# Optimization experiments

Hardware: AMD Instinct MI355X
Metric: run time of the kernel (lower is better)

Reference implementation:

```python
import jax, jax.numpy as jnp
import numpy as np

NEG = -100000000.0  # NOT_POSSIBLE_TRANSITION
B, T, F, NT = 64, 512, 1024, 50
H = NT + 2  # +2 for start/stop tags
START, STOP = H - 2, H - 1


def setup_inputs() -> dict:
    key = jax.random.key(0)
    k0, k1, k2, k3 = jax.random.split(key, 4)
    features = jax.random.normal(k0, (B, T, F), jnp.float32)
    tags = jax.random.randint(k1, (B, T), 0, NT)
    masks = jnp.ones((B, T), jnp.float32)
    W = jax.random.normal(k2, (H, F), jnp.float32) * 0.02  # nn.Linear weight
    b = jnp.zeros((H,), jnp.float32)                        # nn.Linear bias
    transition = jax.random.normal(k3, (H, H), jnp.float32)
    transition = transition.at[START, :].set(NEG).at[:, STOP].set(NEG)
    return dict(features=features, W=W, b=b, transition=transition,
                masks=masks, tags=tags)


def _forward_algorithm(emit, masks, transition):
    # emit: [B,T,H], masks: [B,T]
    b_, _, h = emit.shape
    init = jnp.full((b_, h), NEG, emit.dtype).at[:, START].set(0.0)

    def step(scores, xs):
        emit_t, mask_t = xs  # [B,H], [B]
        # score_t[b, i] = logsumexp_j(scores[b,j] + transition[i,j] + emit_t[b,i])
        s = scores[:, None, :] + transition[None, :, :] + emit_t[:, :, None]
        s = jax.nn.logsumexp(s, axis=-1)
        m = mask_t[:, None]
        scores = s * m + scores * (1.0 - m)
        return scores, None

    scores, _ = jax.lax.scan(step, init, (emit.transpose(1, 0, 2), masks.T))
    return jax.nn.logsumexp(scores + transition[STOP], axis=-1)  # [B]


def _gold_score(emit, tags, masks, transition):
    b_ = emit.shape[0]
    emit_sc = jnp.take_along_axis(emit, tags[:, :, None], axis=2)[:, :, 0]  # [B,T]
    start = jnp.full((b_, 1), START, tags.dtype)
    tags_ext = jnp.concatenate([start, tags], axis=1)  # [B,T+1]
    trans_sc = transition[tags_ext[:, 1:], tags_ext[:, :-1]]  # [B,T]
    last_pos = masks.sum(axis=1).astype(jnp.int32)  # index into tags_ext
    last_tag = jnp.take_along_axis(tags_ext, last_pos[:, None], axis=1)[:, 0]
    last_score = transition[STOP, last_tag]
    return ((trans_sc + emit_sc) * masks).sum(axis=1) + last_score  # [B]


def reference(features, W, b, transition, masks, tags):
    emit = features @ W.T + b  # [B,T,H]
    fwd = _forward_algorithm(emit, masks, transition)
    gold = _gold_score(emit, tags, masks, transition)
    return (fwd - gold).mean()  # CRF NLL loss (scalar)


if __name__ == "__main__":
    print(reference(**setup_inputs()))
```

## Files before the change

### kernel.cpp

```cpp
#include <hip/hip_runtime.h>
#include <hip/hip_bf16.h>
#include <math.h>


#define NEGV   (-100000000.0f)
#define BB     64
#define TT     512
#define FF     1024
#define HH     52
#define HP     64
#define S_START 50
#define S_STOP  51
#define NCH    32
#define CLEN   (TT / NCH)

typedef __bf16 bf16x8 __attribute__((ext_vector_type(8)));
typedef __bf16 bf16x4 __attribute__((ext_vector_type(4)));
typedef float  f32x4  __attribute__((ext_vector_type(4)));

#define WS_CHUNK  0u
#define WS_WBF    33554432u
#define WS_EXPT   33685504u
#define WS_GOLD   33693696u
#define WS_CEXP   33693952u

__global__ __launch_bounds__(256) void k_prep(const float* __restrict__ W,
                                              const float* __restrict__ trans,
                                              __bf16* __restrict__ wbf,
                                              __bf16* __restrict__ expT,
                                              float* __restrict__ gold) {
  int n = blockIdx.x;
  if (n == 0) {
    if (threadIdx.x < BB) gold[threadIdx.x] = 0.0f;
    for (int idx = threadIdx.x; idx < 4096; idx += 256) {
      int m = idx >> 6, k = idx & 63;
      float tv = (k >= HH) ? NEGV : ((m >= HH) ? 0.0f : trans[m * HH + k]);
      expT[idx] = (__bf16)__expf(tv);
    }
  }
  for (int k = threadIdx.x; k < FF; k += 256) {
    float v = (n < HH) ? W[n * FF + k] : 0.0f;
    wbf[n * FF + k] = (__bf16)v;
  }
}

__global__ __launch_bounds__(256, 2) void k_scan(const float* __restrict__ feat,
                                                 const __bf16* __restrict__ wbf,
                                                 const __bf16* __restrict__ expT,
                                                 const float* __restrict__ bias,
                                                 const float* __restrict__ trans,
                                                 const float* __restrict__ masks,
                                                 const int* __restrict__ tags,
                                                 float* __restrict__ chunks,
                                                 float* __restrict__ cexp,
                                                 float* __restrict__ gold) {
  const int tid = threadIdx.x;
  const int wv = tid >> 6;
  const int l  = tid & 63;
  const int lm = l & 15;
  const int q  = l >> 4;
  const int chunk = blockIdx.x * 4 + wv;
  const int b = chunk >> 5, c = chunk & 31;

  __shared__ __align__(16) __bf16 PTall[4][64 * 72];
  __shared__ __align__(16) __bf16 Eall[4][CLEN * 64];
  __bf16* pt = PTall[wv];
  __bf16* el = Eall[wv];

  const float* fbase = feat + ((size_t)(b * TT + c * CLEN)) * FF;
  const float* arow  = fbase + (size_t)lm * FF + q * 8;

  f32x4 apre[4][2];
#pragma unroll
  for (int s = 0; s < 4; ++s)
#pragma unroll
    for (int h = 0; h < 2; ++h)
      apre[s][h] = *(const f32x4*)(arow + s * 32 + h * 4);

  bf16x8 bcur[4];
#pragma unroll
  for (int nt = 0; nt < 4; ++nt)
    bcur[nt] = *(const bf16x8*)(wbf + (size_t)(nt * 16 + lm) * FF + q * 8);

  f32x4 acc[4] = {};

#pragma unroll
  for (int kt = 0; kt < 32; ++kt) {
    const int st = kt & 3;
    bf16x8 af;
#pragma unroll
    for (int j = 0; j < 4; ++j) {
      af[j]     = (__bf16)apre[st][0][j];
      af[4 + j] = (__bf16)apre[st][1][j];
    }
    if (kt + 4 < 32) {
#pragma unroll
      for (int h = 0; h < 2; ++h)
        apre[st][h] = *(const f32x4*)(arow + (kt + 4) * 32 + h * 4);
    }
    bf16x8 bnx[4];
    if (kt + 1 < 32) {
#pragma unroll
      for (int nt = 0; nt < 4; ++nt)
        bnx[nt] = *(const bf16x8*)(wbf + (size_t)(nt * 16 + lm) * FF + (kt + 1) * 32 + q * 8);
    }
#pragma unroll
    for (int nt = 0; nt < 4; ++nt)
      acc[nt] = __builtin_amdgcn_mfma_f32_16x16x32_bf16(af, bcur[nt], acc[nt], 0, 0, 0);
    if (kt + 1 < 32) {
#pragma unroll
      for (int nt = 0; nt < 4; ++nt) bcur[nt] = bnx[nt];
    }
  }

#pragma unroll
  for (int nt = 0; nt < 4; ++nt) {
    int n = nt * 16 + lm;
    float bn = (n < HH) ? bias[n] : 0.0f;
#pragma unroll
    for (int rr = 0; rr < 4; ++rr)
      el[(q * 4 + rr) * 64 + n] = (__bf16)(acc[nt][rr] + bn);
  }

  float mreg = (l < CLEN) ? masks[b * TT + c * CLEN + l] : 1.0f;
  int cur = (l < CLEN) ? tags[b * TT + c * CLEN + l] : 0;
  int prev = __shfl_up(cur, 1);
  if (l == 0) prev = (c == 0) ? S_START : tags[b * TT + c * CLEN - 1];
  float gp = 0.0f;
  if (l < CLEN) {
    float e  = (float)el[l * 64 + cur];
    float tr = trans[cur * HH + prev];
    gp = (e + tr) * mreg;
  }
#pragma unroll
  for (int d = 1; d < 64; d <<= 1) gp += __shfl_xor(gp, d);
  if (l == 0) atomicAdd(&gold[b], gp);

  bf16x8 afrag[4][2];
#pragma unroll
  for (int mt = 0; mt < 4; ++mt)
#pragma unroll
    for (int kk = 0; kk < 2; ++kk)
      afrag[mt][kk] = *(const bf16x8*)&expT[(mt * 16 + lm) * 64 + kk * 32 + q * 8];

  for (int idx = l; idx < 4096; idx += 64) {
    int n = idx >> 6, mm = idx & 63;
    pt[n * 72 + mm] = (__bf16)((n == mm) ? 1.0f : 0.0f);
  }

  int eacc = 0, rpend = 0;
  const float LOG2E = 1.4426950408889634f;

  for (int t = 0; t < CLEN; ++t) {
    float mcur = __shfl(mreg, t);
    if (mcur != 0.0f) {
      float sh = (float)(7 + rpend);
      eacc += 7 + rpend;
      rpend = 0;
      float s[4][4];
#pragma unroll
      for (int mt = 0; mt < 4; ++mt) {
        bf16x4 em4 = *(const bf16x4*)&el[t * 64 + mt * 16 + q * 4];
#pragma unroll
        for (int rr = 0; rr < 4; ++rr)
          s[mt][rr] = __builtin_amdgcn_exp2f(fmaf((float)em4[rr], LOG2E, -sh));
      }

      bf16x8 bfr[2][4];
#pragma unroll
      for (int kk = 0; kk < 2; ++kk)
#pragma unroll
        for (int nt = 0; nt < 4; ++nt)
          bfr[kk][nt] = *(const bf16x8*)&pt[(nt * 16 + lm) * 72 + kk * 32 + q * 8];

      const bool trk = ((t & 7) == 7) && (t != CLEN - 1);
      float lmax = 0.0f;
      f32x4 zero = {};
#pragma unroll
      for (int mt = 0; mt < 4; ++mt) {
#pragma unroll
        for (int nt = 0; nt < 4; ++nt) {
          f32x4 a = __builtin_amdgcn_mfma_f32_16x16x32_bf16(afrag[mt][0], bfr[0][nt], zero, 0, 0, 0);
          a = __builtin_amdgcn_mfma_f32_16x16x32_bf16(afrag[mt][1], bfr[1][nt], a, 0, 0, 0);
          bf16x4 w4;
#pragma unroll
          for (int rr = 0; rr < 4; ++rr) {
            float v = a[rr] * s[mt][rr];
            if (trk) lmax = fmaxf(lmax, v);
            w4[rr] = (__bf16)v;
          }
          *(bf16x4*)&pt[(nt * 16 + lm) * 72 + mt * 16 + q * 4] = w4;
        }
      }
      if (trk) {
#pragma unroll
        for (int d = 1; d < 64; d <<= 1) lmax = fmaxf(lmax, __shfl_xor(lmax, d));
        rpend = ilogbf(lmax);
      }
    }
  }

  f32x4* c4 = (f32x4*)(chunks + (size_t)chunk * 4096);
#pragma unroll
  for (int it = 0; it < 16; ++it) {
    f32x4 v;
#pragma unroll
    for (int jr = 0; jr < 4; ++jr) v[jr] = (float)pt[(it * 4 + jr) * 72 + l];
    c4[it * 64 + l] = v;
  }
  if (l == 0) cexp[chunk] = (float)eacc;
}

__global__ __launch_bounds__(64) void k_combine(const float* __restrict__ chunks,
                                                const float* __restrict__ cexp,
                                                const float* __restrict__ trans,
                                                const float* __restrict__ masks,
                                                const int* __restrict__ tags,
                                                const float* __restrict__ gold,
                                                float* __restrict__ out) {
  const int b = blockIdx.x;
  const int l = threadIdx.x;
  __shared__ float vsh[64];
  float v = (l == S_START) ? 1.0f : 0.0f;
  float esum = 0.0f;
  const float LN2 = 0.6931471805599453f;

  float msum = 0.0f;
  for (int t = l; t < TT; t += 64) msum += masks[b * TT + t];

  f32x4 mb[2][16];
  {
    const f32x4* M = (const f32x4*)(chunks + ((size_t)(b * NCH)) * 4096);
#pragma unroll
    for (int jj = 0; jj < 16; ++jj) mb[0][jj] = M[jj * 64 + l];
  }

#pragma unroll
  for (int cc = 0; cc < NCH; ++cc) {
    vsh[l] = v;
    __syncthreads();
    if (cc + 1 < NCH) {
      const f32x4* Mn = (const f32x4*)(chunks + ((size_t)(b * NCH + cc + 1)) * 4096);
#pragma unroll
      for (int jj = 0; jj < 16; ++jj) mb[(cc + 1) & 1][jj] = Mn[jj * 64 + l];
    }
    f32x4 u4 = {};
#pragma unroll
    for (int jj = 0; jj < 16; ++jj) {
      f32x4 m4 = mb[cc & 1][jj];
      const float* vj = &vsh[jj * 4];
      u4[0] += m4[0] * vj[0];
      u4[1] += m4[1] * vj[1];
      u4[2] += m4[2] * vj[2];
      u4[3] += m4[3] * vj[3];
    }
    float u = (u4[0] + u4[1]) + (u4[2] + u4[3]);
    esum += cexp[b * NCH + cc] * LN2;
    float mxx = u;
#pragma unroll
    for (int d = 1; d < 64; d <<= 1) mxx = fmaxf(mxx, __shfl_xor(mxx, d));
    if (mxx > 0.0f) {
      int ee = ilogbf(mxx);
      u = ldexpf(u, -ee);
      esum += (float)ee * LN2;
    }
    v = u;
    __syncthreads();
  }

  float ts = (l < HH) ? trans[S_STOP * HH + l] : NEGV;
  float contrib = v * __expf(ts);
#pragma unroll
  for (int d = 1; d < 64; d <<= 1) {
    contrib += __shfl_xor(contrib, d);
    msum += __shfl_xor(msum, d);
  }
  if (l == 0) {
    int lp = (int)(msum + 0.5f);
    int lt = (lp == 0) ? S_START : tags[b * TT + lp - 1];
    float goldb = gold[b] + trans[S_STOP * HH + lt];
    float fwd = __logf(contrib) + esum;
    atomicAdd(out, (fwd - goldb) * (1.0f / 64.0f));
  }
}

extern "C" void kernel_launch(void* const* d_in, const int* in_sizes, int n_in,
                              void* d_out, int out_size, void* d_ws, size_t ws_size,
                              hipStream_t stream) {
  (void)in_sizes; (void)n_in; (void)out_size; (void)ws_size;
  const float* feat  = (const float*)d_in[0];
  const float* W     = (const float*)d_in[1];
  const float* bias  = (const float*)d_in[2];
  const float* trans = (const float*)d_in[3];
  const float* masks = (const float*)d_in[4];
  const int*   tags  = (const int*)d_in[5];

  char* ws = (char*)d_ws;
  float*  chunks = (float*)(ws + WS_CHUNK);
  __bf16* wbf    = (__bf16*)(ws + WS_WBF);
  __bf16* expT   = (__bf16*)(ws + WS_EXPT);
  float*  gold   = (float*)(ws + WS_GOLD);
  float*  cexp   = (float*)(ws + WS_CEXP);

  hipMemsetAsync(d_out, 0, sizeof(float), stream);
  k_prep<<<HP, 256, 0, stream>>>(W, trans, wbf, expT, gold);
  k_scan<<<(BB * NCH) / 4, 256, 0, stream>>>(feat, wbf, expT, bias, trans, masks,
                                             tags, chunks, cexp, gold);
  k_combine<<<BB, 64, 0, stream>>>(chunks, cexp, trans, masks, tags, gold, (float*)d_out);
}
```

Measured before the change: 262.5 us.

## Split emission GEMM into its own kernel and store chunk matrices in bf16

Moves the feature-by-weight GEMM out of the scan kernel into a separate k_emit kernel that writes bf16 emissions to workspace, with double-buffered weight prefetch. The scan kernel then loads those emissions, precomputes exp values once into fp32 shared memory, and renormalizes only once, at step 7, instead of every 8 steps. Chunk transfer matrices passed to the combine kernel are stored as bf16, halving that traffic. This trades one extra launch and an emission round trip through memory for a lighter, more parallel scan, and risks some accuracy loss from bf16 chunk storage and the less frequent rescaling.

```diff
diff --git a/kernel.cpp b/kernel.cpp
--- a/kernel.cpp
+++ b/kernel.cpp
@@ -19,10 +19,11 @@
 typedef float  f32x4  __attribute__((ext_vector_type(4)));
 
 #define WS_CHUNK  0u
-#define WS_WBF    33554432u
-#define WS_EXPT   33685504u
-#define WS_GOLD   33693696u
-#define WS_CEXP   33693952u
+#define WS_EMITB  16777216u
+#define WS_WBF    20971520u
+#define WS_EXPT   21102592u
+#define WS_GOLD   21110784u
+#define WS_CEXP   21111040u
 
 __global__ __launch_bounds__(256) void k_prep(const float* __restrict__ W,
                                               const float* __restrict__ trans,
@@ -44,14 +45,78 @@
   }
 }
 
-__global__ __launch_bounds__(256, 2) void k_scan(const float* __restrict__ feat,
+__global__ __launch_bounds__(256, 2) void k_emit(const float* __restrict__ feat,
                                                  const __bf16* __restrict__ wbf,
+                                                 const float* __restrict__ bias,
+                                                 __bf16* __restrict__ emitb) {
+  const int tid = threadIdx.x;
+  const int wv = tid >> 6;
+  const int l  = tid & 63;
+  const int lm = l & 15;
+  const int q  = l >> 4;
+  const size_t row0 = (size_t)blockIdx.x * 64 + wv * 16;
+  const float* arow = feat + (row0 + lm) * FF + q * 8;
+
+  float bn[4];
+#pragma unroll
+  for (int nt = 0; nt < 4; ++nt) {
+    int n = nt * 16 + lm;
+    bn[nt] = (n < HH) ? bias[n] : 0.0f;
+  }
+
+  f32x4 apre[4][2];
+#pragma unroll
+  for (int s = 0; s < 4; ++s)
+#pragma unroll
+    for (int h = 0; h < 2; ++h)
+      apre[s][h] = *(const f32x4*)(arow + s * 32 + h * 4);
+
+  bf16x8 bpre[2][4];
+#pragma unroll
+  for (int sb = 0; sb < 2; ++sb)
+#pragma unroll
+    for (int nt = 0; nt < 4; ++nt)
+      bpre[sb][nt] = *(const bf16x8*)(wbf + (size_t)(nt * 16 + lm) * FF + sb * 32 + q * 8);
+
+  f32x4 acc[4] = {};
+
+#pragma unroll
+  for (int kt = 0; kt < 32; ++kt) {
+    const int st = kt & 3, sb = kt & 1;
+    bf16x8 af;
+#pragma unroll
+    for (int j = 0; j < 4; ++j) {
+      af[j]     = (__bf16)apre[st][0][j];
+      af[4 + j] = (__bf16)apre[st][1][j];
+    }
+#pragma unroll
+    for (int nt = 0; nt < 4; ++nt)
+      acc[nt] = __builtin_amdgcn_mfma_f32_16x16x32_bf16(af, bpre[sb][nt], acc[nt], 0, 0, 0);
+    if (kt + 4 < 32) {
+#pragma unroll
+      for (int h = 0; h < 2; ++h)
+        apre[st][h] = *(const f32x4*)(arow + (kt + 4) * 32 + h * 4);
+    }
+    if (kt + 2 < 32) {
+#pragma unroll
+      for (int nt = 0; nt < 4; ++nt)
+        bpre[sb][nt] = *(const bf16x8*)(wbf + (size_t)(nt * 16 + lm) * FF + (kt + 2) * 32 + q * 8);
+    }
+  }
+
+#pragma unroll
+  for (int nt = 0; nt < 4; ++nt)
+#pragma unroll
+    for (int rr = 0; rr < 4; ++rr)
+      emitb[(row0 + q * 4 + rr) * HP + nt * 16 + lm] = (__bf16)(acc[nt][rr] + bn[nt]);
+}
+
+__global__ __launch_bounds__(256, 2) void k_scan(const __bf16* __restrict__ emitb,
                                                  const __bf16* __restrict__ expT,
-                                                 const float* __restrict__ bias,
                                                  const float* __restrict__ trans,
                                                  const float* __restrict__ masks,
                                                  const int* __restrict__ tags,
-                                                 float* __restrict__ chunks,
+                                                 __bf16* __restrict__ chunks,
                                                  float* __restrict__ cexp,
                                                  float* __restrict__ gold) {
   const int tid = threadIdx.x;
@@ -63,63 +128,38 @@
   const int b = chunk >> 5, c = chunk & 31;
 
   __shared__ __align__(16) __bf16 PTall[4][64 * 72];
-  __shared__ __align__(16) __bf16 Eall[4][CLEN * 64];
+  __shared__ __align__(16) float  Eall[4][CLEN * 64];
   __bf16* pt = PTall[wv];
-  __bf16* el = Eall[wv];
-
-  const float* fbase = feat + ((size_t)(b * TT + c * CLEN)) * FF;
-  const float* arow  = fbase + (size_t)lm * FF + q * 8;
-
-  f32x4 apre[4][2];
-#pragma unroll
-  for (int s = 0; s < 4; ++s)
-#pragma unroll
-    for (int h = 0; h < 2; ++h)
-      apre[s][h] = *(const f32x4*)(arow + s * 32 + h * 4);
-
-  bf16x8 bcur[4];
-#pragma unroll
-  for (int nt = 0; nt < 4; ++nt)
-    bcur[nt] = *(const bf16x8*)(wbf + (size_t)(nt * 16 + lm) * FF + q * 8);
-
-  f32x4 acc[4] = {};
-
-#pragma unroll
-  for (int kt = 0; kt < 32; ++kt) {
-    const int st = kt & 3;
-    bf16x8 af;
-#pragma unroll
-    for (int j = 0; j < 4; ++j) {
-      af[j]     = (__bf16)apre[st][0][j];
-      af[4 + j] = (__bf16)apre[st][1][j];
-    }
-    if (kt + 4 < 32) {
-#pragma unroll
-      for (int h = 0; h < 2; ++h)
-        apre[st][h] = *(const f32x4*)(arow + (kt + 4) * 32 + h * 4);
-    }
-    bf16x8 bnx[4];
-    if (kt + 1 < 32) {
-#pragma unroll
-      for (int nt = 0; nt < 4; ++nt)
-        bnx[nt] = *(const bf16x8*)(wbf + (size_t)(nt * 16 + lm) * FF + (kt + 1) * 32 + q * 8);
-    }
-#pragma unroll
-    for (int nt = 0; nt < 4; ++nt)
-      acc[nt] = __builtin_amdgcn_mfma_f32_16x16x32_bf16(af, bcur[nt], acc[nt], 0, 0, 0);
-    if (kt + 1 < 32) {
-#pragma unroll
-      for (int nt = 0; nt < 4; ++nt) bcur[nt] = bnx[nt];
-    }
-  }
-
-#pragma unroll
-  for (int nt = 0; nt < 4; ++nt) {
-    int n = nt * 16 + lm;
-    float bn = (n < HH) ? bias[n] : 0.0f;
-#pragma unroll
-    for (int rr = 0; rr < 4; ++rr)
-      el[(q * 4 + rr) * 64 + n] = (__bf16)(acc[nt][rr] + bn);
+  float*  E  = Eall[wv];
+
+  const float LOG2E = 1.4426950408889634f;
+  const float LN2   = 0.6931471805599453f;
+
+  const __bf16* tb = emitb + (size_t)(b * TT + c * CLEN) * HP;
+  bf16x8 v0 = *(const bf16x8*)(tb + l * 16);
+  bf16x8 v1 = *(const bf16x8*)(tb + l * 16 + 8);
+  float ev[16];
+#pragma unroll
+  for (int j = 0; j < 8; ++j) {
+    ev[j]     = __builtin_amdgcn_exp2f(fmaf((float)v0[j], LOG2E, -7.0f));
+    ev[8 + j] = __builtin_amdgcn_exp2f(fmaf((float)v1[j], LOG2E, -7.0f));
+  }
+#pragma unroll
+  for (int h = 0; h < 4; ++h) {
+    f32x4 e4 = { ev[h * 4], ev[h * 4 + 1], ev[h * 4 + 2], ev[h * 4 + 3] };
+    *(f32x4*)&E[l * 16 + h * 4] = e4;
+  }
+
+  bf16x8 afrag[4][2];
+#pragma unroll
+  for (int mt = 0; mt < 4; ++mt)
+#pragma unroll
+    for (int kk = 0; kk < 2; ++kk)
+      afrag[mt][kk] = *(const bf16x8*)&expT[(mt * 16 + lm) * 64 + kk * 32 + q * 8];
+
+  for (int idx = l; idx < 4096; idx += 64) {
+    int n = idx >> 6, mm = idx & 63;
+    pt[n * 72 + mm] = (__bf16)((n == mm) ? 1.0f : 0.0f);
   }
 
   float mreg = (l < CLEN) ? masks[b * TT + c * CLEN + l] : 1.0f;
@@ -128,42 +168,26 @@
   if (l == 0) prev = (c == 0) ? S_START : tags[b * TT + c * CLEN - 1];
   float gp = 0.0f;
   if (l < CLEN) {
-    float e  = (float)el[l * 64 + cur];
-    float tr = trans[cur * HH + prev];
-    gp = (e + tr) * mreg;
+    float e = fmaf(__log2f(E[l * 64 + cur]), LN2, 7.0f * LN2);
+    gp = (e + trans[cur * HH + prev]) * mreg;
   }
 #pragma unroll
   for (int d = 1; d < 64; d <<= 1) gp += __shfl_xor(gp, d);
   if (l == 0) atomicAdd(&gold[b], gp);
 
-  bf16x8 afrag[4][2];
-#pragma unroll
-  for (int mt = 0; mt < 4; ++mt)
-#pragma unroll
-    for (int kk = 0; kk < 2; ++kk)
-      afrag[mt][kk] = *(const bf16x8*)&expT[(mt * 16 + lm) * 64 + kk * 32 + q * 8];
-
-  for (int idx = l; idx < 4096; idx += 64) {
-    int n = idx >> 6, mm = idx & 63;
-    pt[n * 72 + mm] = (__bf16)((n == mm) ? 1.0f : 0.0f);
-  }
-
   int eacc = 0, rpend = 0;
-  const float LOG2E = 1.4426950408889634f;
+  float rs = 1.0f;
 
   for (int t = 0; t < CLEN; ++t) {
     float mcur = __shfl(mreg, t);
     if (mcur != 0.0f) {
-      float sh = (float)(7 + rpend);
       eacc += 7 + rpend;
-      rpend = 0;
       float s[4][4];
 #pragma unroll
       for (int mt = 0; mt < 4; ++mt) {
-        bf16x4 em4 = *(const bf16x4*)&el[t * 64 + mt * 16 + q * 4];
-#pragma unroll
-        for (int rr = 0; rr < 4; ++rr)
-          s[mt][rr] = __builtin_amdgcn_exp2f(fmaf((float)em4[rr], LOG2E, -sh));
+        f32x4 e4 = *(const f32x4*)&E[t * 64 + mt * 16 + q * 4];
+#pragma unroll
+        for (int rr = 0; rr < 4; ++rr) s[mt][rr] = e4[rr] * rs;
       }
 
       bf16x8 bfr[2][4];
@@ -173,7 +197,7 @@
         for (int nt = 0; nt < 4; ++nt)
           bfr[kk][nt] = *(const bf16x8*)&pt[(nt * 16 + lm) * 72 + kk * 32 + q * 8];
 
-      const bool trk = ((t & 7) == 7) && (t != CLEN - 1);
+      const bool trk = (t == 7);
       float lmax = 0.0f;
       f32x4 zero = {};
 #pragma unroll
@@ -196,22 +220,26 @@
 #pragma unroll
         for (int d = 1; d < 64; d <<= 1) lmax = fmaxf(lmax, __shfl_xor(lmax, d));
         rpend = ilogbf(lmax);
+        rs = __builtin_amdgcn_exp2f(-(float)rpend);
+      } else {
+        rpend = 0;
+        rs = 1.0f;
       }
     }
   }
 
-  f32x4* c4 = (f32x4*)(chunks + (size_t)chunk * 4096);
-#pragma unroll
-  for (int it = 0; it < 16; ++it) {
-    f32x4 v;
-#pragma unroll
-    for (int jr = 0; jr < 4; ++jr) v[jr] = (float)pt[(it * 4 + jr) * 72 + l];
-    c4[it * 64 + l] = v;
+  __bf16* cb = chunks + (size_t)chunk * 4096;
+#pragma unroll
+  for (int jj = 0; jj < 8; ++jj) {
+    bf16x8 w;
+#pragma unroll
+    for (int e = 0; e < 8; ++e) w[e] = pt[(jj * 8 + e) * 72 + l];
+    *(bf16x8*)(cb + jj * 512 + l * 8) = w;
   }
   if (l == 0) cexp[chunk] = (float)eacc;
 }
 
-__global__ __launch_bounds__(64) void k_combine(const float* __restrict__ chunks,
+__global__ __launch_bounds__(64) void k_combine(const __bf16* __restrict__ chunks,
                                                 const float* __restrict__ cexp,
                                                 const float* __restrict__ trans,
                                                 const float* __restrict__ masks,
@@ -228,11 +256,11 @@
   float msum = 0.0f;
   for (int t = l; t < TT; t += 64) msum += masks[b * TT + t];
 
-  f32x4 mb[2][16];
+  bf16x8 mb[2][8];
   {
-    const f32x4* M = (const f32x4*)(chunks + ((size_t)(b * NCH)) * 4096);
-#pragma unroll
-    for (int jj = 0; jj < 16; ++jj) mb[0][jj] = M[jj * 64 + l];
+    const __bf16* base = chunks + (size_t)(b * NCH) * 4096;
+#pragma unroll
+    for (int jj = 0; jj < 8; ++jj) mb[0][jj] = *(const bf16x8*)(base + jj * 512 + l * 8);
   }
 
 #pragma unroll
@@ -240,21 +268,22 @@
     vsh[l] = v;
     __syncthreads();
     if (cc + 1 < NCH) {
-      const f32x4* Mn = (const f32x4*)(chunks + ((size_t)(b * NCH + cc + 1)) * 4096);
-#pragma unroll
-      for (int jj = 0; jj < 16; ++jj) mb[(cc + 1) & 1][jj] = Mn[jj * 64 + l];
-    }
-    f32x4 u4 = {};
-#pragma unroll
-    for (int jj = 0; jj < 16; ++jj) {
-      f32x4 m4 = mb[cc & 1][jj];
-      const float* vj = &vsh[jj * 4];
-      u4[0] += m4[0] * vj[0];
-      u4[1] += m4[1] * vj[1];
-      u4[2] += m4[2] * vj[2];
-      u4[3] += m4[3] * vj[3];
-    }
-    float u = (u4[0] + u4[1]) + (u4[2] + u4[3]);
+      const __bf16* bn = chunks + (size_t)(b * NCH + cc + 1) * 4096;
+#pragma unroll
+      for (int jj = 0; jj < 8; ++jj) mb[(cc + 1) & 1][jj] = *(const bf16x8*)(bn + jj * 512 + l * 8);
+    }
+    float u0 = 0.f, u1 = 0.f;
+#pragma unroll
+    for (int jj = 0; jj < 8; ++jj) {
+      bf16x8 m8 = mb[cc & 1][jj];
+      const float* vj = &vsh[jj * 8];
+#pragma unroll
+      for (int e = 0; e < 4; ++e) {
+        u0 += (float)m8[e] * vj[e];
+        u1 += (float)m8[4 + e] * vj[4 + e];
+      }
+    }
+    float u = u0 + u1;
     esum += cexp[b * NCH + cc] * LN2;
     float mxx = u;
 #pragma unroll
@@ -296,7 +325,8 @@
   const int*   tags  = (const int*)d_in[5];
 
   char* ws = (char*)d_ws;
-  float*  chunks = (float*)(ws + WS_CHUNK);
+  __bf16* chunks = (__bf16*)(ws + WS_CHUNK);
+  __bf16* emitb  = (__bf16*)(ws + WS_EMITB);
   __bf16* wbf    = (__bf16*)(ws + WS_WBF);
   __bf16* expT   = (__bf16*)(ws + WS_EXPT);
   float*  gold   = (float*)(ws + WS_GOLD);
@@ -304,7 +334,8 @@
 
   hipMemsetAsync(d_out, 0, sizeof(float), stream);
   k_prep<<<HP, 256, 0, stream>>>(W, trans, wbf, expT, gold);
-  k_scan<<<(BB * NCH) / 4, 256, 0, stream>>>(feat, wbf, expT, bias, trans, masks,
-                                             tags, chunks, cexp, gold);
+  k_emit<<<(BB * TT) / 64, 256, 0, stream>>>(feat, wbf, bias, emitb);
+  k_scan<<<(BB * NCH) / 4, 256, 0, stream>>>(emitb, expT, trans, masks, tags,
+                                             chunks, cexp, gold);
   k_combine<<<BB, 64, 0, stream>>>(chunks, cexp, trans, masks, tags, gold, (float*)d_out);
 }
```

Result: slower. 284.5 us (+8.4%).
